# Performance work log

Hardware: AMD Instinct MI355X
Metric: run time of the kernel (lower is better)

The kernel has to match this reference:

```python
import jax, jax.numpy as jnp
import numpy as np

D = 768      # embed_dim
L = 12       # depth
NH = 12      # num_heads
HS = D // NH # head_size = 64
HID = 4 * D  # mlp hidden = 3072
EPS = 1e-5


def setup_inputs() -> dict:
    key = jax.random.key(0)
    ks = jax.random.split(key, 6)
    std = 0.02
    # fix_init_weight rescale: proj.weight and fc2.weight divided by sqrt(2*layer_id)
    rescale = 1.0 / jnp.sqrt(2.0 * jnp.arange(1, L + 1, dtype=jnp.float32))[:, None, None]
    inp = {
        "x": jax.random.normal(ks[0], (2, 1024, D), jnp.float32),
        "Wqkv": jax.random.normal(ks[1], (L, 3 * D, D), jnp.float32) * std,
        "bqkv": jnp.zeros((L, 3 * D), jnp.float32),
        "Wproj": jax.random.normal(ks[2], (L, D, D), jnp.float32) * std * rescale,
        "bproj": jnp.zeros((L, D), jnp.float32),
        "W1": jax.random.normal(ks[3], (L, HID, D), jnp.float32) * std,
        "b1": jnp.zeros((L, HID), jnp.float32),
        "W2": jax.random.normal(ks[4], (L, D, HID), jnp.float32) * std * rescale,
        "b2": jnp.zeros((L, D), jnp.float32),
        "ln1w": jnp.ones((L, D), jnp.float32),
        "ln1b": jnp.zeros((L, D), jnp.float32),
        "ln2w": jnp.ones((L, D), jnp.float32),
        "ln2b": jnp.zeros((L, D), jnp.float32),
        "lnw": jnp.ones((D,), jnp.float32),
        "lnb": jnp.zeros((D,), jnp.float32),
    }
    return inp


def _layernorm(x, w, b):
    mu = x.mean(-1, keepdims=True)
    var = ((x - mu) ** 2).mean(-1, keepdims=True)
    return (x - mu) / jnp.sqrt(var + EPS) * w + b


def _sincos_pos_embed(n, d):
    # get_1d_sincos_pos_embed: omega = 1/10000**(arange(d/2)/(d/2))
    omega = 1.0 / (10000.0 ** (jnp.arange(d // 2, dtype=jnp.float32) / (d / 2.0)))
    out = jnp.arange(n, dtype=jnp.float32)[:, None] * omega[None, :]  # [n, d/2]
    return jnp.concatenate([jnp.sin(out), jnp.cos(out)], axis=1)      # [n, d]


def _forward(x, Wqkv, bqkv, Wproj, bproj, W1, b1, W2, b2,
             ln1w, ln1b, ln2w, ln2b, lnw, lnb):
    b, n, d = x.shape
    x = x + _sincos_pos_embed(n, d)[None]
    scale = HS ** -0.5

    def block(x, p):
        wqkv, bq, wp, bp, w1, b1_, w2, b2_, l1w, l1b, l2w, l2b = p
        # pre-norm attention (mask=False -> plain softmax attention)
        h = _layernorm(x, l1w, l1b)
        qkv = h @ wqkv.T + bq                                   # [b, n, 3d]
        qkv = qkv.reshape(b, n, 3, NH, HS).transpose(2, 0, 3, 1, 4)
        q, k, v = qkv[0], qkv[1], qkv[2]                        # [b, nh, n, hs]
        att = jax.nn.softmax(scale * jnp.einsum('bhqd,bhkd->bhqk', q, k), axis=-1)
        o = jnp.einsum('bhqk,bhkd->bhqd', att, v)               # [b, nh, n, hs]
        o = o.transpose(0, 2, 1, 3).reshape(b, n, d)
        x = x + (o @ wp.T + bp)
        # pre-norm MLP (exact GELU, as nn.GELU default)
        h2 = _layernorm(x, l2w, l2b)
        y = jax.nn.gelu(h2 @ w1.T + b1_, approximate=False) @ w2.T + b2_
        return x + y, None

    x, _ = jax.lax.scan(block, x,
                        (Wqkv, bqkv, Wproj, bproj, W1, b1, W2, b2,
                         ln1w, ln1b, ln2w, ln2b))
    return _layernorm(x, lnw, lnb)


def reference(x, Wqkv, bqkv, Wproj, bproj, W1, b1, W2, b2,
              ln1w, ln1b, ln2w, ln2b, lnw, lnb):
    return _forward(x, Wqkv, bqkv, Wproj, bproj, W1, b1, W2, b2,
                    ln1w, ln1b, ln2w, ln2b, lnw, lnb)
```

## Files before the change

### kernel.cpp

```cpp
#include <hip/hip_runtime.h>
#include <math.h>

#define NTOK 2048
#define DM 768
#define NHD 12
#define HS 64
#define SEQ 1024
#define HID 3072
#define NL 12

typedef __attribute__((ext_vector_type(8))) short short8;
typedef __attribute__((ext_vector_type(4))) float f32x4;
typedef __attribute__((ext_vector_type(4))) unsigned short us4;
typedef unsigned short u16;

static __device__ __forceinline__ u16 f2bf(float f) {
    unsigned u = __float_as_uint(f);
    u = (u + 0x7fffu + ((u >> 16) & 1u)) >> 16;
    return (u16)u;
}

static __device__ __forceinline__ void gload16(const void* g, void* l) {
    __builtin_amdgcn_global_load_lds(
        (const __attribute__((address_space(1))) void*)g,
        (__attribute__((address_space(3))) void*)l,
        16, 0, 0);
}

__global__ void posadd_k(const float* __restrict__ xin, float* __restrict__ xout) {
    int idx = blockIdx.x * 256 + threadIdx.x;
    int d = idx % DM;
    int tok = (idx / DM) & (SEQ - 1);
    int i = (d < 384) ? d : d - 384;
    float omega = expf((float)i * (-9.210340371976184f / 384.0f));
    float ang = (float)tok * omega;
    float pe = (d < 384) ? sinf(ang) : cosf(ang);
    xout[idx] = xin[idx] + pe;
}

__global__ void cvt_k(const float* __restrict__ in, u16* __restrict__ out) {
    int idx = blockIdx.x * 256 + threadIdx.x;
    float4 f = ((const float4*)in)[idx];
    us4 u = { f2bf(f.x), f2bf(f.y), f2bf(f.z), f2bf(f.w) };
    ((us4*)out)[idx] = u;
}

template<bool OUTBF>
__global__ __launch_bounds__(256) void ln_k(
        const float* __restrict__ x, const float* __restrict__ w,
        const float* __restrict__ b, void* __restrict__ out) {
    int l = threadIdx.x & 63, wv = threadIdx.x >> 6;
    int row = blockIdx.x * 4 + wv;
    const float* xr = x + (size_t)row * DM;
    float4 v[3];
#pragma unroll
    for (int c = 0; c < 3; c++) v[c] = *(const float4*)(xr + c * 256 + l * 4);
    float s = 0.f;
#pragma unroll
    for (int c = 0; c < 3; c++) s += v[c].x + v[c].y + v[c].z + v[c].w;
#pragma unroll
    for (int off = 32; off; off >>= 1) s += __shfl_xor(s, off, 64);
    float mu = s * (1.0f / DM);
    float vs = 0.f;
#pragma unroll
    for (int c = 0; c < 3; c++) {
        float dx;
        dx = v[c].x - mu; vs += dx * dx;
        dx = v[c].y - mu; vs += dx * dx;
        dx = v[c].z - mu; vs += dx * dx;
        dx = v[c].w - mu; vs += dx * dx;
    }
#pragma unroll
    for (int off = 32; off; off >>= 1) vs += __shfl_xor(vs, off, 64);
    float rstd = rsqrtf(vs * (1.0f / DM) + 1e-5f);
#pragma unroll
    for (int c = 0; c < 3; c++) {
        float4 w4 = *(const float4*)(w + c * 256 + l * 4);
        float4 b4 = *(const float4*)(b + c * 256 + l * 4);
        float y0 = (v[c].x - mu) * rstd * w4.x + b4.x;
        float y1 = (v[c].y - mu) * rstd * w4.y + b4.y;
        float y2 = (v[c].z - mu) * rstd * w4.z + b4.z;
        float y3 = (v[c].w - mu) * rstd * w4.w + b4.w;
        if (OUTBF) {
            us4 u = { f2bf(y0), f2bf(y1), f2bf(y2), f2bf(y3) };
            *(us4*)((u16*)out + (size_t)row * DM + c * 256 + l * 4) = u;
        } else {
            float4 o4 = { y0, y1, y2, y3 };
            *(float4*)((float*)out + (size_t)row * DM + c * 256 + l * 4) = o4;
        }
    }
}

template<int BM, int BN, int NT, int WR, int WC, int MODE>
__global__ __launch_bounds__(NT) void gemm_k(
        const u16* __restrict__ A, const u16* __restrict__ B,
        const float* __restrict__ bias, int K,
        float* __restrict__ xres, u16* __restrict__ o0, u16* __restrict__ o1,
        u16* __restrict__ o2) {
    constexpr int WM = BM / WR, WN = BN / WC;
    constexpr int FM = WM / 16, FN = WN / 16;
    constexpr int ACH = (BM * 128) / (NT * 16);
    constexpr int BCH = (BN * 128) / (NT * 16);

    __shared__ u16 lA[2][BM * 64];
    __shared__ u16 lB[2][BN * 64];
    const char* Ab = (const char*)A;
    const char* Bb = (const char*)B;

    int tid = threadIdx.x;
    int l = tid & 63, w = tid >> 6;
    int lr = l & 15, lg = l >> 4;
    int wr = w / WC, wc = w % WC;

    int gx = gridDim.x, gy = gridDim.y;
    int nwg = gx * gy;
    int flat = blockIdx.y * gx + blockIdx.x;
    int virt = (flat & 7) * (nwg >> 3) + (flat >> 3);
    int bx = virt / gy;
    int by = virt % gy;
    int bm = by * BM;
    int bn = bx * BN;

    auto stage = [&](int buf, int kk) {
#pragma unroll
        for (int c = 0; c < ACH; c++) {
            int p = (c * NT + tid) * 16;
            int row = p >> 7, kb = p & 127;
            int kbs = kb ^ ((row & 7) << 4);
            gload16(Ab + ((size_t)(bm + row) * K + kk) * 2 + kbs, (char*)lA[buf] + p);
        }
#pragma unroll
        for (int c = 0; c < BCH; c++) {
            int p = (c * NT + tid) * 16;
            int row = p >> 7, kb = p & 127;
            int kbs = kb ^ ((row & 7) << 4);
            gload16(Bb + ((size_t)(bn + row) * K + kk) * 2 + kbs, (char*)lB[buf] + p);
        }
    };

    f32x4 acc[FM][FN] = {};

    stage(0, 0);
    __syncthreads();
    int cur = 0;
    for (int kk = 0; kk < K; kk += 64) {
        if (kk + 64 < K) stage(cur ^ 1, kk + 64);
        const char* lAb = (const char*)lA[cur];
        const char* lBb = (const char*)lB[cur];
#pragma unroll
        for (int ks = 0; ks < 2; ks++) {
            short8 af[FM], bf[FN];
#pragma unroll
            for (int i = 0; i < FM; i++) {
                int row = wr * WM + i * 16 + lr;
                int kb = ks * 64 + lg * 16;
                af[i] = *(const short8*)(lAb + row * 128 + (kb ^ ((row & 7) << 4)));
            }
#pragma unroll
            for (int j = 0; j < FN; j++) {
                int row = wc * WN + j * 16 + lr;
                int kb = ks * 64 + lg * 16;
                bf[j] = *(const short8*)(lBb + row * 128 + (kb ^ ((row & 7) << 4)));
            }
#pragma unroll
            for (int i = 0; i < FM; i++)
#pragma unroll
                for (int j = 0; j < FN; j++)
                    acc[i][j] = __builtin_amdgcn_mfma_f32_16x16x32_bf16(af[i], bf[j], acc[i][j], 0, 0, 0);
        }
        __syncthreads();
        cur ^= 1;
    }

#pragma unroll
    for (int i = 0; i < FM; i++)
#pragma unroll
        for (int j = 0; j < FN; j++)
#pragma unroll
            for (int r = 0; r < 4; r++) {
                int gm = bm + wr * WM + i * 16 + lg * 4 + r;
                int gn = bn + wc * WN + j * 16 + lr;
                float v = acc[i][j][r] + bias[gn];
                if (MODE == 0) {
                    int bi = gm >> 10, tok = gm & (SEQ - 1);
                    int which = gn / DM;
                    int wi = gn - which * DM;
                    int h = wi >> 6, d = wi & 63;
                    if (which == 0)      o0[(((size_t)bi * NHD + h) * SEQ + tok) * HS + d] = f2bf(v * 0.125f);
                    else if (which == 1) o1[(((size_t)bi * NHD + h) * SEQ + tok) * HS + d] = f2bf(v);
                    else                 o2[(((size_t)bi * NHD + h) * HS + d) * SEQ + tok] = f2bf(v);
                } else if (MODE == 1) {
                    size_t ix = (size_t)gm * DM + gn;
                    xres[ix] += v;
                } else {
                    float g = 0.5f * v * (1.0f + erff(v * 0.70710678f));
                    o0[(size_t)gm * HID + gn] = f2bf(g);
                }
            }
}

__global__ __launch_bounds__(256) void attn_k(
        const u16* __restrict__ q, const u16* __restrict__ k,
        const u16* __restrict__ vtg, float* __restrict__ Of,
        float* __restrict__ ml) {
    __shared__ u16 kt[2][64 * 64];
    __shared__ u16 vtile[2][64 * 64];
    __shared__ u16 plds[4][16][72];

    int tid = threadIdx.x;
    int l = tid & 63, w = tid >> 6;
    int lr = l & 15, lg = l >> 4;

    int flat = (blockIdx.z * gridDim.y + blockIdx.y) * gridDim.x + blockIdx.x;
    int virt = (flat & 7) * 96 + (flat >> 3);
    int bh = virt >> 5;
    int rem = virt & 31;
    int half = rem >> 4;
    int qb = rem & 15;

    int qbase = qb * 64 + w * 16;
    int kv0 = half * (SEQ / 2);

    const u16* qp = q + (size_t)bh * SEQ * HS;
    const char* kp = (const char*)(k + (size_t)bh * SEQ * HS);
    const char* vp = (const char*)(vtg + (size_t)bh * HS * SEQ);

    short8 aq[2];
#pragma unroll
    for (int c = 0; c < 2; c++)
        aq[c] = *(const short8*)(qp + (size_t)(qbase + lr) * HS + c * 32 + lg * 8);

    auto stage = [&](int buf, int kb) {
#pragma unroll
        for (int c = 0; c < 2; c++) {
            int p = (c * 256 + tid) * 16;
            int row = p >> 7, db = p & 127;
            int dbs = db ^ ((row & 7) << 4);
            gload16(kp + (size_t)(kb + row) * 128 + dbs, (char*)kt[buf] + p);
        }
#pragma unroll
        for (int c = 0; c < 2; c++) {
            int p = (c * 256 + tid) * 16;
            int row = p >> 7, db = p & 127;
            int dbs = db ^ ((row & 7) << 4);
            gload16(vp + (size_t)row * (SEQ * 2) + kb * 2 + dbs, (char*)vtile[buf] + p);
        }
    };

    float mrow[4], lsum[4];
#pragma unroll
    for (int r = 0; r < 4; r++) { mrow[r] = -1e30f; lsum[r] = 0.f; }
    f32x4 oacc[4] = {};

    stage(0, kv0);
    __syncthreads();
    int buf = 0;
    for (int kb = kv0; kb < kv0 + SEQ / 2; kb += 64) {
        if (kb + 64 < kv0 + SEQ / 2) stage(buf ^ 1, kb + 64);
        const char* kb_ = (const char*)kt[buf];
        const char* vb_ = (const char*)vtile[buf];

        f32x4 s[4];
        __builtin_amdgcn_s_setprio(1);
#pragma unroll
        for (int t = 0; t < 4; t++) {
            f32x4 st = {};
#pragma unroll
            for (int c = 0; c < 2; c++) {
                int row = t * 16 + lr;
                short8 bk = *(const short8*)(kb_ + row * 128 + ((c * 64 + lg * 16) ^ ((row & 7) << 4)));
                st = __builtin_amdgcn_mfma_f32_16x16x32_bf16(aq[c], bk, st, 0, 0, 0);
            }
            s[t] = st;
        }
        __builtin_amdgcn_s_setprio(0);

        float e[4][4], scl[4];
#pragma unroll
        for (int r = 0; r < 4; r++) {
            float mx = fmaxf(fmaxf(s[0][r], s[1][r]), fmaxf(s[2][r], s[3][r]));
#pragma unroll
            for (int off = 8; off; off >>= 1) mx = fmaxf(mx, __shfl_xor(mx, off, 16));
            float mnew = fmaxf(mrow[r], mx);
            float sc = __expf(mrow[r] - mnew);
            float ss = 0.f;
#pragma unroll
            for (int t = 0; t < 4; t++) { e[t][r] = __expf(s[t][r] - mnew); ss += e[t][r]; }
#pragma unroll
            for (int off = 8; off; off >>= 1) ss += __shfl_xor(ss, off, 16);
            lsum[r] = lsum[r] * sc + ss;
            mrow[r] = mnew;
            scl[r] = sc;
        }
#pragma unroll
        for (int j = 0; j < 4; j++)
#pragma unroll
            for (int r = 0; r < 4; r++) oacc[j][r] *= scl[r];

#pragma unroll
        for (int t = 0; t < 4; t++)
#pragma unroll
            for (int r = 0; r < 4; r++)
                plds[w][lg * 4 + r][t * 16 + lr] = f2bf(e[t][r]);
        short8 pa[2];
#pragma unroll
        for (int kc = 0; kc < 2; kc++)
            pa[kc] = *(const short8*)(&plds[w][lr][kc * 32 + lg * 8]);

        __builtin_amdgcn_s_setprio(1);
#pragma unroll
        for (int j = 0; j < 4; j++) {
            int row = j * 16 + lr;
#pragma unroll
            for (int kc = 0; kc < 2; kc++) {
                short8 bv = *(const short8*)(vb_ + row * 128 + ((kc * 64 + lg * 16) ^ ((row & 7) << 4)));
                oacc[j] = __builtin_amdgcn_mfma_f32_16x16x32_bf16(pa[kc], bv, oacc[j], 0, 0, 0);
            }
        }
        __builtin_amdgcn_s_setprio(0);
        __syncthreads();
        buf ^= 1;
    }

    size_t pbase = ((size_t)(bh * 2 + half) * SEQ);
#pragma unroll
    for (int j = 0; j < 4; j++)
#pragma unroll
        for (int r = 0; r < 4; r++) {
            int qrow = qbase + lg * 4 + r;
            Of[(pbase + qrow) * 64 + j * 16 + lr] = oacc[j][r];
        }
    if (lr == 0) {
#pragma unroll
        for (int r = 0; r < 4; r++) {
            int qrow = qbase + lg * 4 + r;
            ((float2*)ml)[pbase + qrow] = make_float2(mrow[r], lsum[r]);
        }
    }
}

__global__ __launch_bounds__(256) void attncomb_k(
        const float* __restrict__ Of, const float* __restrict__ ml,
        u16* __restrict__ o) {
    int gid = blockIdx.x * 256 + threadIdx.x;
    int row = gid >> 4;
    int dc = (gid & 15) * 4;
    int bh = row >> 10, qrow = row & 1023;
    int bi = bh / NHD, h = bh - bi * NHD;
    const float2* mlp = (const float2*)ml;
    float2 ml0 = mlp[(size_t)(bh * 2 + 0) * SEQ + qrow];
    float2 ml1 = mlp[(size_t)(bh * 2 + 1) * SEQ + qrow];
    float m = fmaxf(ml0.x, ml1.x);
    float e0 = __expf(ml0.x - m), e1 = __expf(ml1.x - m);
    float rl = 1.0f / (ml0.y * e0 + ml1.y * e1);
    float4 o0 = *(const float4*)(Of + ((size_t)(bh * 2 + 0) * SEQ + qrow) * 64 + dc);
    float4 o1 = *(const float4*)(Of + ((size_t)(bh * 2 + 1) * SEQ + qrow) * 64 + dc);
    us4 u;
    u[0] = f2bf((o0.x * e0 + o1.x * e1) * rl);
    u[1] = f2bf((o0.y * e0 + o1.y * e1) * rl);
    u[2] = f2bf((o0.z * e0 + o1.z * e1) * rl);
    u[3] = f2bf((o0.w * e0 + o1.w * e1) * rl);
    *(us4*)(o + ((size_t)(bi * SEQ + qrow) * DM) + h * HS + dc) = u;
}

extern "C" void kernel_launch(void* const* d_in, const int* in_sizes, int n_in,
                              void* d_out, int out_size, void* d_ws, size_t ws_size,
                              hipStream_t stream) {
    const float* x_in  = (const float*)d_in[0];
    const float* Wqkv  = (const float*)d_in[1];
    const float* bqkv  = (const float*)d_in[2];
    const float* Wproj = (const float*)d_in[3];
    const float* bproj = (const float*)d_in[4];
    const float* W1    = (const float*)d_in[5];
    const float* b1    = (const float*)d_in[6];
    const float* W2    = (const float*)d_in[7];
    const float* b2    = (const float*)d_in[8];
    const float* ln1w  = (const float*)d_in[9];
    const float* ln1b  = (const float*)d_in[10];
    const float* ln2w  = (const float*)d_in[11];
    const float* ln2b  = (const float*)d_in[12];
    const float* lnw   = (const float*)d_in[13];
    const float* lnb   = (const float*)d_in[14];

    char* ws = (char*)d_ws;
    size_t off = 0;
    auto alloc = [&](size_t bytes) -> void* {
        void* p = ws + off;
        off += (bytes + 255) & ~(size_t)255;
        return p;
    };
    float* xbuf = (float*)alloc((size_t)NTOK * DM * 4);
    u16* hbuf   = (u16*)alloc((size_t)NTOK * DM * 2);
    u16* qb     = (u16*)alloc((size_t)2 * NHD * SEQ * HS * 2);
    u16* kb     = (u16*)alloc((size_t)2 * NHD * SEQ * HS * 2);
    u16* vtb    = (u16*)alloc((size_t)2 * NHD * SEQ * HS * 2);
    u16* ob     = (u16*)alloc((size_t)NTOK * DM * 2);
    u16* h2b    = (u16*)alloc((size_t)NTOK * HID * 2);
    float* Of   = (float*)alloc((size_t)24 * 2 * SEQ * 64 * 4);
    float* mlb  = (float*)alloc((size_t)24 * 2 * SEQ * 8);

    const size_t nWqkv  = (size_t)NL * 3 * DM * DM;
    const size_t nWproj = (size_t)NL * DM * DM;
    const size_t nW1    = (size_t)NL * HID * DM;
    const size_t nW2    = (size_t)NL * DM * HID;
    size_t wbytes = (nWqkv + nWproj + nW1 + nW2) * 2 + 4 * 256;
    bool wb = (off + wbytes) <= ws_size;

    u16 *wqkvh = nullptr, *wprojh = nullptr, *w1h = nullptr, *w2h = nullptr;
    u16 *cvtbuf = nullptr;
    if (wb) {
        wqkvh  = (u16*)alloc(nWqkv * 2);
        wprojh = (u16*)alloc(nWproj * 2);
        w1h    = (u16*)alloc(nW1 * 2);
        w2h    = (u16*)alloc(nW2 * 2);
    } else {
        cvtbuf = (u16*)alloc((size_t)HID * DM * 2);
    }

    posadd_k<<<dim3((NTOK * DM) / 256), 256, 0, stream>>>(x_in, xbuf);
    if (wb) {
        cvt_k<<<dim3((unsigned)(nWqkv / 4 / 256)), 256, 0, stream>>>(Wqkv, wqkvh);
        cvt_k<<<dim3((unsigned)(nWproj / 4 / 256)), 256, 0, stream>>>(Wproj, wprojh);
        cvt_k<<<dim3((unsigned)(nW1 / 4 / 256)), 256, 0, stream>>>(W1, w1h);
        cvt_k<<<dim3((unsigned)(nW2 / 4 / 256)), 256, 0, stream>>>(W2, w2h);
    }

    for (int l = 0; l < NL; l++) {
        const u16* wqkv_l;
        const u16* wproj_l;
        const u16* w1_l;
        const u16* w2_l;

        ln_k<true><<<dim3(NTOK / 4), 256, 0, stream>>>(xbuf, ln1w + l * DM, ln1b + l * DM, hbuf);

        if (wb) wqkv_l = wqkvh + (size_t)l * 3 * DM * DM;
        else {
            cvt_k<<<dim3(3 * DM * DM / 1024), 256, 0, stream>>>(Wqkv + (size_t)l * 3 * DM * DM, cvtbuf);
            wqkv_l = cvtbuf;
        }
        gemm_k<128, 64, 256, 2, 2, 0><<<dim3(3 * DM / 64, NTOK / 128), 256, 0, stream>>>(
            hbuf, wqkv_l, bqkv + (size_t)l * 3 * DM, DM, nullptr, qb, kb, vtb);

        attn_k<<<dim3(SEQ / 64, 24, 2), 256, 0, stream>>>(qb, kb, vtb, Of, mlb);
        attncomb_k<<<dim3(24 * SEQ * 16 / 256), 256, 0, stream>>>(Of, mlb, ob);

        if (wb) wproj_l = wprojh + (size_t)l * DM * DM;
        else {
            cvt_k<<<dim3(DM * DM / 1024), 256, 0, stream>>>(Wproj + (size_t)l * DM * DM, cvtbuf);
            wproj_l = cvtbuf;
        }
        gemm_k<64, 64, 256, 2, 2, 1><<<dim3(DM / 64, NTOK / 64), 256, 0, stream>>>(
            ob, wproj_l, bproj + (size_t)l * DM, DM, xbuf, nullptr, nullptr, nullptr);

        ln_k<true><<<dim3(NTOK / 4), 256, 0, stream>>>(xbuf, ln2w + l * DM, ln2b + l * DM, hbuf);

        if (wb) w1_l = w1h + (size_t)l * HID * DM;
        else {
            cvt_k<<<dim3(HID * DM / 1024), 256, 0, stream>>>(W1 + (size_t)l * HID * DM, cvtbuf);
            w1_l = cvtbuf;
        }
        gemm_k<128, 64, 256, 2, 2, 2><<<dim3(HID / 64, NTOK / 128), 256, 0, stream>>>(
            hbuf, w1_l, b1 + (size_t)l * HID, DM, nullptr, h2b, nullptr, nullptr);

        if (wb) w2_l = w2h + (size_t)l * DM * HID;
        else {
            cvt_k<<<dim3(DM * HID / 1024), 256, 0, stream>>>(W2 + (size_t)l * DM * HID, cvtbuf);
            w2_l = cvtbuf;
        }
        gemm_k<64, 64, 256, 2, 2, 1><<<dim3(DM / 64, NTOK / 64), 256, 0, stream>>>(
            h2b, w2_l, b2 + (size_t)l * DM, HID, xbuf, nullptr, nullptr, nullptr);
    }

    ln_k<false><<<dim3(NTOK / 4), 256, 0, stream>>>(xbuf, lnw, lnb, (float*)d_out);
}
```

Measured before the change: 1.691 ms.

## Split-K the projection and MLP-down GEMMs with a separate reduction kernel

The output-projection GEMM (K=768) and the fc2 GEMM (K=3072) are split along K into 2 and 4 slices across blockIdx.z. Each slice writes fp32 partial sums to a workspace, and a new reduction kernel adds the partials, the bias and the residual. This raises the number of workgroups for these narrow-N GEMMs (384 base tiles) to fill more CUs. In exchange it adds extra global traffic for the partial buffers (up to 4x NTOK*DM fp32) and one more launch per GEMM.

```diff
diff --git a/kernel.cpp b/kernel.cpp
--- a/kernel.cpp
+++ b/kernel.cpp
@@ -94,9 +94,9 @@
 template<int BM, int BN, int NT, int WR, int WC, int MODE>
 __global__ __launch_bounds__(NT) void gemm_k(
         const u16* __restrict__ A, const u16* __restrict__ B,
-        const float* __restrict__ bias, int K,
+        const float* __restrict__ bias, int K, int Kld,
         float* __restrict__ xres, u16* __restrict__ o0, u16* __restrict__ o1,
-        u16* __restrict__ o2) {
+        u16* __restrict__ o2, float* __restrict__ cp) {
     constexpr int WM = BM / WR, WN = BN / WC;
     constexpr int FM = WM / 16, FN = WN / 16;
     constexpr int ACH = (BM * 128) / (NT * 16);
@@ -104,8 +104,6 @@
 
     __shared__ u16 lA[2][BM * 64];
     __shared__ u16 lB[2][BN * 64];
-    const char* Ab = (const char*)A;
-    const char* Bb = (const char*)B;
 
     int tid = threadIdx.x;
     int l = tid & 63, w = tid >> 6;
@@ -121,20 +119,25 @@
     int bm = by * BM;
     int bn = bx * BN;
 
+    int koff = (MODE == 3) ? blockIdx.z * K : 0;
+    const char* Ab = (const char*)A + (size_t)koff * 2;
+    const char* Bb = (const char*)B + (size_t)koff * 2;
+    float* cpb = (MODE == 3) ? cp + (size_t)blockIdx.z * NTOK * DM : nullptr;
+
     auto stage = [&](int buf, int kk) {
 #pragma unroll
         for (int c = 0; c < ACH; c++) {
             int p = (c * NT + tid) * 16;
             int row = p >> 7, kb = p & 127;
             int kbs = kb ^ ((row & 7) << 4);
-            gload16(Ab + ((size_t)(bm + row) * K + kk) * 2 + kbs, (char*)lA[buf] + p);
+            gload16(Ab + ((size_t)(bm + row) * Kld + kk) * 2 + kbs, (char*)lA[buf] + p);
         }
 #pragma unroll
         for (int c = 0; c < BCH; c++) {
             int p = (c * NT + tid) * 16;
             int row = p >> 7, kb = p & 127;
             int kbs = kb ^ ((row & 7) << 4);
-            gload16(Bb + ((size_t)(bn + row) * K + kk) * 2 + kbs, (char*)lB[buf] + p);
+            gload16(Bb + ((size_t)(bn + row) * Kld + kk) * 2 + kbs, (char*)lB[buf] + p);
         }
     };
 
@@ -180,6 +183,10 @@
             for (int r = 0; r < 4; r++) {
                 int gm = bm + wr * WM + i * 16 + lg * 4 + r;
                 int gn = bn + wc * WN + j * 16 + lr;
+                if (MODE == 3) {
+                    cpb[(size_t)gm * DM + gn] = acc[i][j][r];
+                    continue;
+                }
                 float v = acc[i][j][r] + bias[gn];
                 if (MODE == 0) {
                     int bi = gm >> 10, tok = gm & (SEQ - 1);
@@ -197,6 +204,24 @@
                     o0[(size_t)gm * HID + gn] = f2bf(g);
                 }
             }
+}
+
+template<int SK>
+__global__ __launch_bounds__(256) void skred_k(
+        const float* __restrict__ cp, const float* __restrict__ bias,
+        float* __restrict__ xres) {
+    int gid = blockIdx.x * 256 + threadIdx.x;
+    int col4 = gid % (DM / 4);
+    float4 b4 = ((const float4*)bias)[col4];
+    float4 s = b4;
+#pragma unroll
+    for (int p = 0; p < SK; p++) {
+        float4 v = ((const float4*)cp)[(size_t)p * (NTOK * DM / 4) + gid];
+        s.x += v.x; s.y += v.y; s.z += v.z; s.w += v.w;
+    }
+    float4 x4 = ((float4*)xres)[gid];
+    x4.x += s.x; x4.y += s.y; x4.z += s.z; x4.w += s.w;
+    ((float4*)xres)[gid] = x4;
 }
 
 __global__ __launch_bounds__(256) void attn_k(
@@ -398,6 +423,7 @@
     u16* h2b    = (u16*)alloc((size_t)NTOK * HID * 2);
     float* Of   = (float*)alloc((size_t)24 * 2 * SEQ * 64 * 4);
     float* mlb  = (float*)alloc((size_t)24 * 2 * SEQ * 8);
+    float* skbuf= (float*)alloc((size_t)4 * NTOK * DM * 4);
 
     const size_t nWqkv  = (size_t)NL * 3 * DM * DM;
     const size_t nWproj = (size_t)NL * DM * DM;
@@ -439,7 +465,8 @@
             wqkv_l = cvtbuf;
         }
         gemm_k<128, 64, 256, 2, 2, 0><<<dim3(3 * DM / 64, NTOK / 128), 256, 0, stream>>>(
-            hbuf, wqkv_l, bqkv + (size_t)l * 3 * DM, DM, nullptr, qb, kb, vtb);
+            hbuf, wqkv_l, bqkv + (size_t)l * 3 * DM, DM, DM,
+            nullptr, qb, kb, vtb, nullptr);
 
         attn_k<<<dim3(SEQ / 64, 24, 2), 256, 0, stream>>>(qb, kb, vtb, Of, mlb);
         attncomb_k<<<dim3(24 * SEQ * 16 / 256), 256, 0, stream>>>(Of, mlb, ob);
@@ -449,8 +476,11 @@
             cvt_k<<<dim3(DM * DM / 1024), 256, 0, stream>>>(Wproj + (size_t)l * DM * DM, cvtbuf);
             wproj_l = cvtbuf;
         }
-        gemm_k<64, 64, 256, 2, 2, 1><<<dim3(DM / 64, NTOK / 64), 256, 0, stream>>>(
-            ob, wproj_l, bproj + (size_t)l * DM, DM, xbuf, nullptr, nullptr, nullptr);
+        gemm_k<64, 64, 256, 2, 2, 3><<<dim3(DM / 64, NTOK / 64, 2), 256, 0, stream>>>(
+            ob, wproj_l, nullptr, DM / 2, DM,
+            nullptr, nullptr, nullptr, nullptr, skbuf);
+        skred_k<2><<<dim3(NTOK * DM / 4 / 256), 256, 0, stream>>>(
+            skbuf, bproj + (size_t)l * DM, xbuf);
 
         ln_k<true><<<dim3(NTOK / 4), 256, 0, stream>>>(xbuf, ln2w + l * DM, ln2b + l * DM, hbuf);
 
@@ -460,15 +490,19 @@
             w1_l = cvtbuf;
         }
         gemm_k<128, 64, 256, 2, 2, 2><<<dim3(HID / 64, NTOK / 128), 256, 0, stream>>>(
-            hbuf, w1_l, b1 + (size_t)l * HID, DM, nullptr, h2b, nullptr, nullptr);
+            hbuf, w1_l, b1 + (size_t)l * HID, DM, DM,
+            nullptr, h2b, nullptr, nullptr, nullptr);
 
         if (wb) w2_l = w2h + (size_t)l * DM * HID;
         else {
             cvt_k<<<dim3(DM * HID / 1024), 256, 0, stream>>>(W2 + (size_t)l * DM * HID, cvtbuf);
             w2_l = cvtbuf;
         }
-        gemm_k<64, 64, 256, 2, 2, 1><<<dim3(DM / 64, NTOK / 64), 256, 0, stream>>>(
-            h2b, w2_l, b2 + (size_t)l * DM, HID, xbuf, nullptr, nullptr, nullptr);
+        gemm_k<64, 64, 256, 2, 2, 3><<<dim3(DM / 64, NTOK / 64, 4), 256, 0, stream>>>(
+            h2b, w2_l, nullptr, HID / 4, HID,
+            nullptr, nullptr, nullptr, nullptr, skbuf);
+        skred_k<4><<<dim3(NTOK * DM / 4 / 256), 256, 0, stream>>>(
+            skbuf, b2 + (size_t)l * DM, xbuf);
     }
 
     ln_k<false><<<dim3(NTOK / 4), 256, 0, stream>>>(xbuf, lnw, lnb, (float*)d_out);
```

After: 1.691 ms. Within noise of the previous version (+0.0%).
